# Performance work log

Measured on AMD Instinct MI355X. Metric: run time of the kernel, lower is better.

The kernel has to match this reference:

```python
import jax, jax.numpy as jnp
import numpy as np

K, D, N, T, B = 8, 16, 32, 200, 2048
_LOG2PI = float(np.log(2.0 * np.pi))


def setup_inputs() -> dict:
    key = jax.random.key(0)
    ks = jax.random.split(key, 13)
    return {
        "discrete_states": jax.random.randint(ks[0], (B, T), 0, K),
        "continuous_states": jax.random.normal(ks[1], (B, T, D), dtype=jnp.float32),
        "obs": jax.random.normal(ks[2], (B, T, N), dtype=jnp.float32),
        "discrete_init_logits": jax.random.normal(ks[3], (K,), dtype=jnp.float32),
        "continuous_init_locs": jax.random.normal(ks[4], (K, D), dtype=jnp.float32),
        "continuous_init_log_scales": jax.random.normal(ks[5], (K, D), dtype=jnp.float32),
        "state_transition_logits": jax.random.normal(ks[6], (K, K), dtype=jnp.float32),
        "dynamics_matrices": jax.random.normal(ks[7], (K, D, D), dtype=jnp.float32) * 0.3,
        "dynamics_offsets": jax.random.normal(ks[8], (K, D), dtype=jnp.float32),
        # NOTE: original code uses dynamics_log_scales directly as a scale (missing .exp());
        # we keep that math faithfully but init it strictly positive to stay finite.
        "dynamics_log_scales": jax.random.uniform(ks[9], (K, D), minval=0.5, maxval=1.5, dtype=jnp.float32),
        "emission_matrices": jax.random.normal(ks[10], (K, N, D), dtype=jnp.float32),
        "emission_offsets": jax.random.normal(ks[11], (K, N), dtype=jnp.float32),
        "emission_log_scales": jax.random.normal(ks[12], (K, N), dtype=jnp.float32),
    }


def _normal_lp(x, loc, scale):
    # elementwise Normal log-prob
    return -0.5 * jnp.square((x - loc) / scale) - jnp.log(scale) - 0.5 * _LOG2PI


def reference(discrete_states, continuous_states, obs,
              discrete_init_logits, continuous_init_locs, continuous_init_log_scales,
              state_transition_logits, dynamics_matrices, dynamics_offsets,
              dynamics_log_scales, emission_matrices, emission_offsets,
              emission_log_scales):
    """log p(s_{1:T}, z_{1:T}, x_{1:T}) -> [B]"""
    s0 = discrete_states[:, 0]                      # [B]
    z0 = continuous_states[:, 0]                    # [B,D]
    # p(s_1)
    lp = jax.nn.log_softmax(discrete_init_logits)[s0]
    # p(z_1 | s_1)
    lp = lp + _normal_lp(z0, continuous_init_locs[s0],
                         jnp.exp(continuous_init_log_scales[s0])).sum(-1)
    # p(s_t | s_{t-1}) for t=2..T, fully vectorized over time
    s_prev = discrete_states[:, :-1]
    s_cur = discrete_states[:, 1:]
    trans = jax.nn.log_softmax(state_transition_logits, axis=-1)  # [K,K]
    lp = lp + trans[s_prev, s_cur].sum(-1)
    # p(z_t | z_{t-1}, s_t)
    A = dynamics_matrices[s_cur]                    # [B,T-1,D,D] gather
    dyn_loc = jnp.einsum('btij,btj->bti', A, continuous_states[:, :-1]) + dynamics_offsets[s_cur]
    dyn_scale = dynamics_log_scales[s_cur]          # faithful: original omits .exp()
    lp = lp + _normal_lp(continuous_states[:, 1:], dyn_loc, dyn_scale).sum((-1, -2))
    # p(x_t | z_t, s_t) for all t
    C = emission_matrices[discrete_states]          # [B,T,N,D] gather
    em_loc = jnp.einsum('btij,btj->bti', C, continuous_states) + emission_offsets[discrete_states]
    em_scale = jnp.exp(emission_log_scales[discrete_states])
    lp = lp + _normal_lp(obs, em_loc, em_scale).sum((-1, -2))
    return lp
```

## Files before the change

kernel.cpp:

```cpp
#include <hip/hip_runtime.h>

#define KK 8
#define DD 16
#define NN 32
#define TT 200
#define BB 2048

#define SC 516
#define SA 260
#define SE 36
#define SD 20

__device__ __forceinline__ float dot16(const float* __restrict__ row,
                                       const float* __restrict__ z) {
  const float4* r4 = reinterpret_cast<const float4*>(row);
  float4 c0 = r4[0], c1 = r4[1], c2 = r4[2], c3 = r4[3];
  float a = c0.x * z[0], b = c0.y * z[1];
  a = fmaf(c0.z, z[2], a);  b = fmaf(c0.w, z[3], b);
  a = fmaf(c1.x, z[4], a);  b = fmaf(c1.y, z[5], b);
  a = fmaf(c1.z, z[6], a);  b = fmaf(c1.w, z[7], b);
  a = fmaf(c2.x, z[8], a);  b = fmaf(c2.y, z[9], b);
  a = fmaf(c2.z, z[10], a); b = fmaf(c2.w, z[11], b);
  a = fmaf(c3.x, z[12], a); b = fmaf(c3.y, z[13], b);
  a = fmaf(c3.z, z[14], a); b = fmaf(c3.w, z[15], b);
  return a + b;
}

__global__ __launch_bounds__(256) void slds_lp_kernel(
    const int* __restrict__ dsts,
    const float* __restrict__ zg,
    const float* __restrict__ obsg,
    const float* __restrict__ initlg,
    const float* __restrict__ initloc,
    const float* __restrict__ initls,
    const float* __restrict__ transg,
    const float* __restrict__ Ag,
    const float* __restrict__ dynoff,
    const float* __restrict__ dynls,
    const float* __restrict__ Cg,
    const float* __restrict__ emoff,
    const float* __restrict__ emls,
    float* __restrict__ out)
{
  __shared__ __align__(16) float sC[KK * SC];
  __shared__ __align__(16) float sA[KK * SA];
  __shared__ __align__(16) float sEmOff[KK * SE];
  __shared__ __align__(16) float sEmInv[KK * SE];
  __shared__ __align__(16) float sDynOff[KK * SD];
  __shared__ __align__(16) float sDynInv[KK * SD];
  __shared__ __align__(16) float sInitLoc[KK * SD];
  __shared__ __align__(16) float sInitInv[KK * SD];
  __shared__ float sTrans[KK * KK];
  __shared__ float sEmConst[KK];
  __shared__ float sDynConst[KK];
  __shared__ float sInitLp[KK];

  const float HALF_LOG2PI = 0.91893853320467274178f;
  const int tid = threadIdx.x;

  for (int i = tid; i < KK * NN * DD; i += 256) {
    int k = i >> 9, r = i & 511;
    sC[k * SC + r] = Cg[i];
  }
  for (int i = tid; i < KK * DD * DD; i += 256) {
    int k = i >> 8, r = i & 255;
    sA[k * SA + r] = Ag[i];
  }
  if (tid < KK * NN) {
    int k = tid >> 5, n = tid & 31;
    sEmOff[k * SE + n] = emoff[tid];
    sEmInv[k * SE + n] = expf(-emls[tid]);
  }
  if (tid < KK * DD) {
    int k = tid >> 4, d = tid & 15;
    sDynOff[k * SD + d] = dynoff[tid];
    sDynInv[k * SD + d] = 1.0f / dynls[tid];
    sInitLoc[k * SD + d] = initloc[tid];
    sInitInv[k * SD + d] = expf(-initls[tid]);
  }
  if (tid < KK * KK) {
    int kr = tid >> 3;
    float mx = transg[kr * KK];
    for (int j = 1; j < KK; ++j) mx = fmaxf(mx, transg[kr * KK + j]);
    float ss = 0.f;
    for (int j = 0; j < KK; ++j) ss += expf(transg[kr * KK + j] - mx);
    sTrans[tid] = transg[tid] - (logf(ss) + mx);
  }
  if (tid < KK) {
    int k = tid;
    float se = 0.f;
    for (int n = 0; n < NN; ++n) se -= emls[k * NN + n];
    sEmConst[k] = se - NN * HALF_LOG2PI;
    float sd = 0.f;
    for (int d = 0; d < DD; ++d) sd -= logf(dynls[k * DD + d]);
    sDynConst[k] = sd - DD * HALF_LOG2PI;
    float mx = initlg[0];
    for (int j = 1; j < KK; ++j) mx = fmaxf(mx, initlg[j]);
    float ss = 0.f;
    for (int j = 0; j < KK; ++j) ss += expf(initlg[j] - mx);
    float si = 0.f;
    for (int d = 0; d < DD; ++d) si -= initls[k * DD + d];
    sInitLp[k] = initlg[k] - (logf(ss) + mx) + si - DD * HALF_LOG2PI;
  }
  __syncthreads();

  const int nItems = BB * TT;
  const int gstride = gridDim.x * blockDim.x;
  for (int item = blockIdx.x * blockDim.x + tid; item < nItems; item += gstride) {
    const int b = item / TT;
    const int t = item - b * TT;

    float z[16];
    {
      const float4* p = reinterpret_cast<const float4*>(zg + (size_t)item * DD);
      float4 a0 = p[0], a1 = p[1], a2 = p[2], a3 = p[3];
      z[0] = a0.x; z[1] = a0.y; z[2] = a0.z; z[3] = a0.w;
      z[4] = a1.x; z[5] = a1.y; z[6] = a1.z; z[7] = a1.w;
      z[8] = a2.x; z[9] = a2.y; z[10] = a2.z; z[11] = a2.w;
      z[12] = a3.x; z[13] = a3.y; z[14] = a3.z; z[15] = a3.w;
    }
    const int s = dsts[item];

    const float4* o4 = reinterpret_cast<const float4*>(obsg + (size_t)item * NN);
    const int cb = s * SC;
    const int eb4 = s * (SE / 4);
    float acc = 0.f;
#pragma unroll 2
    for (int g = 0; g < 8; ++g) {
      float4 o = o4[g];
      float4 off = reinterpret_cast<const float4*>(sEmOff)[eb4 + g];
      float4 inv = reinterpret_cast<const float4*>(sEmInv)[eb4 + g];
      int n0 = g * 4;
      float l0 = dot16(&sC[cb + (n0 + 0) * DD], z) + off.x;
      float l1 = dot16(&sC[cb + (n0 + 1) * DD], z) + off.y;
      float l2 = dot16(&sC[cb + (n0 + 2) * DD], z) + off.z;
      float l3 = dot16(&sC[cb + (n0 + 3) * DD], z) + off.w;
      float d0 = (o.x - l0) * inv.x;
      float d1 = (o.y - l1) * inv.y;
      float d2 = (o.z - l2) * inv.z;
      float d3 = (o.w - l3) * inv.w;
      acc = fmaf(d0, d0, acc); acc = fmaf(d1, d1, acc);
      acc = fmaf(d2, d2, acc); acc = fmaf(d3, d3, acc);
    }
    float lp = -0.5f * acc + sEmConst[s];

    if (t != 0) {
      const int sp = dsts[item - 1];
      float zp[16];
      {
        const float4* p = reinterpret_cast<const float4*>(zg + (size_t)(item - 1) * DD);
        float4 a0 = p[0], a1 = p[1], a2 = p[2], a3 = p[3];
        zp[0] = a0.x; zp[1] = a0.y; zp[2] = a0.z; zp[3] = a0.w;
        zp[4] = a1.x; zp[5] = a1.y; zp[6] = a1.z; zp[7] = a1.w;
        zp[8] = a2.x; zp[9] = a2.y; zp[10] = a2.z; zp[11] = a2.w;
        zp[12] = a3.x; zp[13] = a3.y; zp[14] = a3.z; zp[15] = a3.w;
      }
      const int ab = s * SA;
      const int db4 = s * (SD / 4);
      float a2acc = 0.f;
#pragma unroll 2
      for (int g = 0; g < 4; ++g) {
        float4 off = reinterpret_cast<const float4*>(sDynOff)[db4 + g];
        float4 inv = reinterpret_cast<const float4*>(sDynInv)[db4 + g];
        int i0 = g * 4;
        float l0 = dot16(&sA[ab + (i0 + 0) * DD], zp) + off.x;
        float l1 = dot16(&sA[ab + (i0 + 1) * DD], zp) + off.y;
        float l2 = dot16(&sA[ab + (i0 + 2) * DD], zp) + off.z;
        float l3 = dot16(&sA[ab + (i0 + 3) * DD], zp) + off.w;
        float d0 = (z[i0 + 0] - l0) * inv.x;
        float d1 = (z[i0 + 1] - l1) * inv.y;
        float d2 = (z[i0 + 2] - l2) * inv.z;
        float d3 = (z[i0 + 3] - l3) * inv.w;
        a2acc = fmaf(d0, d0, a2acc); a2acc = fmaf(d1, d1, a2acc);
        a2acc = fmaf(d2, d2, a2acc); a2acc = fmaf(d3, d3, a2acc);
      }
      lp += -0.5f * a2acc + sDynConst[s] + sTrans[sp * KK + s];
    } else {
      const int ib4 = s * (SD / 4);
      float a2acc = 0.f;
#pragma unroll 2
      for (int g = 0; g < 4; ++g) {
        float4 loc = reinterpret_cast<const float4*>(sInitLoc)[ib4 + g];
        float4 inv = reinterpret_cast<const float4*>(sInitInv)[ib4 + g];
        int i0 = g * 4;
        float d0 = (z[i0 + 0] - loc.x) * inv.x;
        float d1 = (z[i0 + 1] - loc.y) * inv.y;
        float d2 = (z[i0 + 2] - loc.z) * inv.z;
        float d3 = (z[i0 + 3] - loc.w) * inv.w;
        a2acc = fmaf(d0, d0, a2acc); a2acc = fmaf(d1, d1, a2acc);
        a2acc = fmaf(d2, d2, a2acc); a2acc = fmaf(d3, d3, a2acc);
      }
      lp += -0.5f * a2acc + sInitLp[s];
    }

    const int lane = tid & 63;
    float v = lp;
#pragma unroll
    for (int off = 1; off < 64; off <<= 1) {
      float ov = __shfl_up(v, off, 64);
      int obk = __shfl_up(b, off, 64);
      if (lane >= off && obk == b) v += ov;
    }
    int nb = __shfl_down(b, 1, 64);
    if (lane == 63 || nb != b) atomicAdd(&out[b], v);
  }
}

extern "C" void kernel_launch(void* const* d_in, const int* in_sizes, int n_in,
                              void* d_out, int out_size, void* d_ws, size_t ws_size,
                              hipStream_t stream) {
  const int*   dsts    = (const int*)d_in[0];
  const float* zg      = (const float*)d_in[1];
  const float* obsg    = (const float*)d_in[2];
  const float* initlg  = (const float*)d_in[3];
  const float* initloc = (const float*)d_in[4];
  const float* initls  = (const float*)d_in[5];
  const float* transg  = (const float*)d_in[6];
  const float* Ag      = (const float*)d_in[7];
  const float* dynoff  = (const float*)d_in[8];
  const float* dynls   = (const float*)d_in[9];
  const float* Cg      = (const float*)d_in[10];
  const float* emoff   = (const float*)d_in[11];
  const float* emls    = (const float*)d_in[12];
  float* out = (float*)d_out;

  hipMemsetAsync(d_out, 0, BB * sizeof(float), stream);

  slds_lp_kernel<<<1600, 256, 0, stream>>>(dsts, zg, obsg, initlg, initloc,
                                           initls, transg, Ag, dynoff, dynls,
                                           Cg, emoff, emls, out);
}
```

Baseline: 143.4 us.

## Process two consecutive timesteps per thread and drop grid-stride loop

Each thread now handles a pair of adjacent timesteps, sharing the loaded z vectors between the dynamics and emission terms and halving thread count (800 blocks of 256 cover exactly B*T/2 pairs). The emission loop interleaves two independent dot-product chains for more ILP, and the grid-stride loop is removed. This lowers the per-block shared-memory preload cost relative to useful work and halves the warp-reduction and atomic overhead, at the cost of higher register pressure and fewer total waves.

```diff
diff --git a/kernel.cpp b/kernel.cpp
--- a/kernel.cpp
+++ b/kernel.cpp
@@ -24,6 +24,16 @@
   a = fmaf(c3.x, z[12], a); b = fmaf(c3.y, z[13], b);
   a = fmaf(c3.z, z[14], a); b = fmaf(c3.w, z[15], b);
   return a + b;
+}
+
+__device__ __forceinline__ void load16(float* __restrict__ d,
+                                       const float* __restrict__ s) {
+  const float4* p = reinterpret_cast<const float4*>(s);
+  float4 a0 = p[0], a1 = p[1], a2 = p[2], a3 = p[3];
+  d[0] = a0.x;  d[1] = a0.y;  d[2] = a0.z;  d[3] = a0.w;
+  d[4] = a1.x;  d[5] = a1.y;  d[6] = a1.z;  d[7] = a1.w;
+  d[8] = a2.x;  d[9] = a2.y;  d[10] = a2.z; d[11] = a2.w;
+  d[12] = a3.x; d[13] = a3.y; d[14] = a3.z; d[15] = a3.w;
 }
 
 __global__ __launch_bounds__(256) void slds_lp_kernel(
@@ -104,106 +114,138 @@
   }
   __syncthreads();
 
-  const int nItems = BB * TT;
-  const int gstride = gridDim.x * blockDim.x;
-  for (int item = blockIdx.x * blockDim.x + tid; item < nItems; item += gstride) {
-    const int b = item / TT;
-    const int t = item - b * TT;
-
-    float z[16];
-    {
-      const float4* p = reinterpret_cast<const float4*>(zg + (size_t)item * DD);
-      float4 a0 = p[0], a1 = p[1], a2 = p[2], a3 = p[3];
-      z[0] = a0.x; z[1] = a0.y; z[2] = a0.z; z[3] = a0.w;
-      z[4] = a1.x; z[5] = a1.y; z[6] = a1.z; z[7] = a1.w;
-      z[8] = a2.x; z[9] = a2.y; z[10] = a2.z; z[11] = a2.w;
-      z[12] = a3.x; z[13] = a3.y; z[14] = a3.z; z[15] = a3.w;
+  const int p = blockIdx.x * 256 + tid;
+  const int b = p / 100;
+  const int tp = p - b * 100;
+  const int item0 = b * TT + (tp << 1);
+
+  const int2 s01 = *reinterpret_cast<const int2*>(dsts + item0);
+  const int s0 = s01.x, s1 = s01.y;
+  const int prevItem = (tp != 0) ? (item0 - 1) : item0;
+  const int sp = dsts[prevItem];
+
+  float z0[16], z1[16], zp[16];
+  load16(z0, zg + (size_t)item0 * DD);
+  load16(z1, zg + (size_t)(item0 + 1) * DD);
+  load16(zp, zg + (size_t)prevItem * DD);
+
+  float lp;
+  {
+    const int a1b = s1 * SA;
+    const int d14 = s1 * (SD / 4);
+    float accD = 0.f, accE = 0.f;
+    if (tp != 0) {
+      const int a0b = s0 * SA;
+      const int d04 = s0 * (SD / 4);
+#pragma unroll
+      for (int g = 0; g < 4; ++g) {
+        const int i0 = g * 4;
+        float4 off1 = reinterpret_cast<const float4*>(sDynOff)[d14 + g];
+        float4 inv1 = reinterpret_cast<const float4*>(sDynInv)[d14 + g];
+        float4 off0 = reinterpret_cast<const float4*>(sDynOff)[d04 + g];
+        float4 inv0 = reinterpret_cast<const float4*>(sDynInv)[d04 + g];
+        float m0 = dot16(&sA[a1b + (i0 + 0) * DD], z0) + off1.x;
+        float m1 = dot16(&sA[a1b + (i0 + 1) * DD], z0) + off1.y;
+        float m2 = dot16(&sA[a1b + (i0 + 2) * DD], z0) + off1.z;
+        float m3 = dot16(&sA[a1b + (i0 + 3) * DD], z0) + off1.w;
+        float n0 = dot16(&sA[a0b + (i0 + 0) * DD], zp) + off0.x;
+        float n1 = dot16(&sA[a0b + (i0 + 1) * DD], zp) + off0.y;
+        float n2 = dot16(&sA[a0b + (i0 + 2) * DD], zp) + off0.z;
+        float n3 = dot16(&sA[a0b + (i0 + 3) * DD], zp) + off0.w;
+        float e0 = (z1[i0 + 0] - m0) * inv1.x;
+        float e1 = (z1[i0 + 1] - m1) * inv1.y;
+        float e2 = (z1[i0 + 2] - m2) * inv1.z;
+        float e3 = (z1[i0 + 3] - m3) * inv1.w;
+        float f0 = (z0[i0 + 0] - n0) * inv0.x;
+        float f1 = (z0[i0 + 1] - n1) * inv0.y;
+        float f2 = (z0[i0 + 2] - n2) * inv0.z;
+        float f3 = (z0[i0 + 3] - n3) * inv0.w;
+        accD = fmaf(e0, e0, accD); accD = fmaf(e1, e1, accD);
+        accD = fmaf(e2, e2, accD); accD = fmaf(e3, e3, accD);
+        accE = fmaf(f0, f0, accE); accE = fmaf(f1, f1, accE);
+        accE = fmaf(f2, f2, accE); accE = fmaf(f3, f3, accE);
+      }
+      lp = -0.5f * (accD + accE) + sDynConst[s1] + sDynConst[s0]
+           + sTrans[s0 * KK + s1] + sTrans[sp * KK + s0];
+    } else {
+      const int i04 = s0 * (SD / 4);
+#pragma unroll
+      for (int g = 0; g < 4; ++g) {
+        const int i0 = g * 4;
+        float4 off1 = reinterpret_cast<const float4*>(sDynOff)[d14 + g];
+        float4 inv1 = reinterpret_cast<const float4*>(sDynInv)[d14 + g];
+        float4 loc = reinterpret_cast<const float4*>(sInitLoc)[i04 + g];
+        float4 iv  = reinterpret_cast<const float4*>(sInitInv)[i04 + g];
+        float m0 = dot16(&sA[a1b + (i0 + 0) * DD], z0) + off1.x;
+        float m1 = dot16(&sA[a1b + (i0 + 1) * DD], z0) + off1.y;
+        float m2 = dot16(&sA[a1b + (i0 + 2) * DD], z0) + off1.z;
+        float m3 = dot16(&sA[a1b + (i0 + 3) * DD], z0) + off1.w;
+        float e0 = (z1[i0 + 0] - m0) * inv1.x;
+        float e1 = (z1[i0 + 1] - m1) * inv1.y;
+        float e2 = (z1[i0 + 2] - m2) * inv1.z;
+        float e3 = (z1[i0 + 3] - m3) * inv1.w;
+        float f0 = (z0[i0 + 0] - loc.x) * iv.x;
+        float f1 = (z0[i0 + 1] - loc.y) * iv.y;
+        float f2 = (z0[i0 + 2] - loc.z) * iv.z;
+        float f3 = (z0[i0 + 3] - loc.w) * iv.w;
+        accD = fmaf(e0, e0, accD); accD = fmaf(e1, e1, accD);
+        accD = fmaf(e2, e2, accD); accD = fmaf(e3, e3, accD);
+        accE = fmaf(f0, f0, accE); accE = fmaf(f1, f1, accE);
+        accE = fmaf(f2, f2, accE); accE = fmaf(f3, f3, accE);
+      }
+      lp = -0.5f * (accD + accE) + sDynConst[s1]
+           + sTrans[s0 * KK + s1] + sInitLp[s0];
     }
-    const int s = dsts[item];
-
-    const float4* o4 = reinterpret_cast<const float4*>(obsg + (size_t)item * NN);
-    const int cb = s * SC;
-    const int eb4 = s * (SE / 4);
-    float acc = 0.f;
-#pragma unroll 2
+  }
+
+  {
+    const float4* oA = reinterpret_cast<const float4*>(obsg + (size_t)item0 * NN);
+    const int c0 = s0 * SC, c1 = s1 * SC;
+    const int e04 = s0 * (SE / 4), e14 = s1 * (SE / 4);
+    float accA = 0.f, accB = 0.f;
+#pragma unroll 1
     for (int g = 0; g < 8; ++g) {
-      float4 o = o4[g];
-      float4 off = reinterpret_cast<const float4*>(sEmOff)[eb4 + g];
-      float4 inv = reinterpret_cast<const float4*>(sEmInv)[eb4 + g];
-      int n0 = g * 4;
-      float l0 = dot16(&sC[cb + (n0 + 0) * DD], z) + off.x;
-      float l1 = dot16(&sC[cb + (n0 + 1) * DD], z) + off.y;
-      float l2 = dot16(&sC[cb + (n0 + 2) * DD], z) + off.z;
-      float l3 = dot16(&sC[cb + (n0 + 3) * DD], z) + off.w;
-      float d0 = (o.x - l0) * inv.x;
-      float d1 = (o.y - l1) * inv.y;
-      float d2 = (o.z - l2) * inv.z;
-      float d3 = (o.w - l3) * inv.w;
-      acc = fmaf(d0, d0, acc); acc = fmaf(d1, d1, acc);
-      acc = fmaf(d2, d2, acc); acc = fmaf(d3, d3, acc);
+      float4 o0 = oA[g];
+      float4 o1 = oA[8 + g];
+      float4 offA = reinterpret_cast<const float4*>(sEmOff)[e04 + g];
+      float4 invA = reinterpret_cast<const float4*>(sEmInv)[e04 + g];
+      float4 offB = reinterpret_cast<const float4*>(sEmOff)[e14 + g];
+      float4 invB = reinterpret_cast<const float4*>(sEmInv)[e14 + g];
+      const int n0 = g * 4;
+      float l0 = dot16(&sC[c0 + (n0 + 0) * DD], z0) + offA.x;
+      float l1 = dot16(&sC[c0 + (n0 + 1) * DD], z0) + offA.y;
+      float l2 = dot16(&sC[c0 + (n0 + 2) * DD], z0) + offA.z;
+      float l3 = dot16(&sC[c0 + (n0 + 3) * DD], z0) + offA.w;
+      float k0 = dot16(&sC[c1 + (n0 + 0) * DD], z1) + offB.x;
+      float k1 = dot16(&sC[c1 + (n0 + 1) * DD], z1) + offB.y;
+      float k2 = dot16(&sC[c1 + (n0 + 2) * DD], z1) + offB.z;
+      float k3 = dot16(&sC[c1 + (n0 + 3) * DD], z1) + offB.w;
+      float d0 = (o0.x - l0) * invA.x;
+      float d1 = (o0.y - l1) * invA.y;
+      float d2 = (o0.z - l2) * invA.z;
+      float d3 = (o0.w - l3) * invA.w;
+      float g0 = (o1.x - k0) * invB.x;
+      float g1 = (o1.y - k1) * invB.y;
+      float g2 = (o1.z - k2) * invB.z;
+      float g3 = (o1.w - k3) * invB.w;
+      accA = fmaf(d0, d0, accA); accA = fmaf(d1, d1, accA);
+      accA = fmaf(d2, d2, accA); accA = fmaf(d3, d3, accA);
+      accB = fmaf(g0, g0, accB); accB = fmaf(g1, g1, accB);
+      accB = fmaf(g2, g2, accB); accB = fmaf(g3, g3, accB);
     }
-    float lp = -0.5f * acc + sEmConst[s];
-
-    if (t != 0) {
-      const int sp = dsts[item - 1];
-      float zp[16];
-      {
-        const float4* p = reinterpret_cast<const float4*>(zg + (size_t)(item - 1) * DD);
-        float4 a0 = p[0], a1 = p[1], a2 = p[2], a3 = p[3];
-        zp[0] = a0.x; zp[1] = a0.y; zp[2] = a0.z; zp[3] = a0.w;
-        zp[4] = a1.x; zp[5] = a1.y; zp[6] = a1.z; zp[7] = a1.w;
-        zp[8] = a2.x; zp[9] = a2.y; zp[10] = a2.z; zp[11] = a2.w;
-        zp[12] = a3.x; zp[13] = a3.y; zp[14] = a3.z; zp[15] = a3.w;
-      }
-      const int ab = s * SA;
-      const int db4 = s * (SD / 4);
-      float a2acc = 0.f;
-#pragma unroll 2
-      for (int g = 0; g < 4; ++g) {
-        float4 off = reinterpret_cast<const float4*>(sDynOff)[db4 + g];
-        float4 inv = reinterpret_cast<const float4*>(sDynInv)[db4 + g];
-        int i0 = g * 4;
-        float l0 = dot16(&sA[ab + (i0 + 0) * DD], zp) + off.x;
-        float l1 = dot16(&sA[ab + (i0 + 1) * DD], zp) + off.y;
-        float l2 = dot16(&sA[ab + (i0 + 2) * DD], zp) + off.z;
-        float l3 = dot16(&sA[ab + (i0 + 3) * DD], zp) + off.w;
-        float d0 = (z[i0 + 0] - l0) * inv.x;
-        float d1 = (z[i0 + 1] - l1) * inv.y;
-        float d2 = (z[i0 + 2] - l2) * inv.z;
-        float d3 = (z[i0 + 3] - l3) * inv.w;
-        a2acc = fmaf(d0, d0, a2acc); a2acc = fmaf(d1, d1, a2acc);
-        a2acc = fmaf(d2, d2, a2acc); a2acc = fmaf(d3, d3, a2acc);
-      }
-      lp += -0.5f * a2acc + sDynConst[s] + sTrans[sp * KK + s];
-    } else {
-      const int ib4 = s * (SD / 4);
-      float a2acc = 0.f;
-#pragma unroll 2
-      for (int g = 0; g < 4; ++g) {
-        float4 loc = reinterpret_cast<const float4*>(sInitLoc)[ib4 + g];
-        float4 inv = reinterpret_cast<const float4*>(sInitInv)[ib4 + g];
-        int i0 = g * 4;
-        float d0 = (z[i0 + 0] - loc.x) * inv.x;
-        float d1 = (z[i0 + 1] - loc.y) * inv.y;
-        float d2 = (z[i0 + 2] - loc.z) * inv.z;
-        float d3 = (z[i0 + 3] - loc.w) * inv.w;
-        a2acc = fmaf(d0, d0, a2acc); a2acc = fmaf(d1, d1, a2acc);
-        a2acc = fmaf(d2, d2, a2acc); a2acc = fmaf(d3, d3, a2acc);
-      }
-      lp += -0.5f * a2acc + sInitLp[s];
-    }
-
-    const int lane = tid & 63;
-    float v = lp;
+    lp += -0.5f * (accA + accB) + sEmConst[s0] + sEmConst[s1];
+  }
+
+  const int lane = tid & 63;
+  float v = lp;
 #pragma unroll
-    for (int off = 1; off < 64; off <<= 1) {
-      float ov = __shfl_up(v, off, 64);
-      int obk = __shfl_up(b, off, 64);
-      if (lane >= off && obk == b) v += ov;
-    }
-    int nb = __shfl_down(b, 1, 64);
-    if (lane == 63 || nb != b) atomicAdd(&out[b], v);
-  }
+  for (int off = 1; off < 64; off <<= 1) {
+    float ov = __shfl_up(v, off, 64);
+    int obk = __shfl_up(b, off, 64);
+    if (lane >= off && obk == b) v += ov;
+  }
+  int nb = __shfl_down(b, 1, 64);
+  if (lane == 63 || nb != b) atomicAdd(&out[b], v);
 }
 
 extern "C" void kernel_launch(void* const* d_in, const int* in_sizes, int n_in,
@@ -226,7 +268,7 @@
 
   hipMemsetAsync(d_out, 0, BB * sizeof(float), stream);
 
-  slds_lp_kernel<<<1600, 256, 0, stream>>>(dsts, zg, obsg, initlg, initloc,
-                                           initls, transg, Ag, dynoff, dynls,
-                                           Cg, emoff, emls, out);
-}
+  slds_lp_kernel<<<800, 256, 0, stream>>>(dsts, zg, obsg, initlg, initloc,
+                                          initls, transg, Ag, dynoff, dynls,
+                                          Cg, emoff, emls, out);
+}
```

Result: slower. 167.9 us (+17.1%).
